# Performance work log

Measured on AMD Instinct MI355X. Metric: run time of the kernel, lower is better.

The kernel has to match this reference:

```python
import jax, jax.numpy as jnp
import numpy as np
from jax import lax

EPS = 1e-5

# ---- 1-bit activation quantizer with straight-through estimator ----
@jax.custom_vjp
def ste_sign(x):
    return jnp.sign(x)

def _ste_sign_fwd(x):
    return jnp.sign(x), x

def _ste_sign_bwd(res, g):
    x = res
    # clipped STE: pass gradient where |x| <= 1
    return (g * (jnp.abs(x) <= 1.0).astype(g.dtype),)

ste_sign.defvjp(_ste_sign_fwd, _ste_sign_bwd)

# ---- 1-bit weight binarization: sign(w) * per-out-channel mean(|w|), STE ----
@jax.custom_vjp
def bin_weight(w):
    alpha = jnp.mean(jnp.abs(w), axis=(1, 2, 3), keepdims=True)  # [O,1,1,1]
    return jnp.sign(w) * alpha

def _bw_fwd(w):
    return bin_weight(w), w

def _bw_bwd(res, g):
    w = res
    # weight_clip=1: straight-through inside the clip range
    return (g * (jnp.abs(w) <= 1.0).astype(g.dtype),)

bin_weight.defvjp(_bw_fwd, _bw_bwd)

def conv3x3(x, w):
    # zero padding=1, stride=1, NCHW / OIHW
    return lax.conv_general_dilated(
        x, w, window_strides=(1, 1), padding=((1, 1), (1, 1)),
        dimension_numbers=('NCHW', 'OIHW', 'NCHW'))

def batchnorm(x, gamma, beta):
    # training-mode BN with batch statistics over (N,H,W)
    mean = jnp.mean(x, axis=(0, 2, 3), keepdims=True)
    var = jnp.var(x, axis=(0, 2, 3), keepdims=True)
    xn = (x - mean) * lax.rsqrt(var + EPS)
    return xn * gamma[None, :, None, None] + beta[None, :, None, None]


def setup_inputs() -> dict:
    key = jax.random.key(0)
    k1, k2, k3 = jax.random.split(key, 3)
    N, C, H, W = 32, 256, 56, 56
    return {
        'x': jax.random.normal(k1, (N, C, H, W), dtype=jnp.float32),
        'w1': jax.random.normal(k2, (C, C, 3, 3), dtype=jnp.float32) * 0.05,
        'gamma1': jnp.ones((C,), dtype=jnp.float32),
        'beta1': jnp.zeros((C,), dtype=jnp.float32),
        'w2': jax.random.normal(k3, (C, C, 3, 3), dtype=jnp.float32) * 0.05,
        'gamma2': jnp.ones((C,), dtype=jnp.float32),
        'beta2': jnp.zeros((C,), dtype=jnp.float32),
    }


def reference(x, w1, gamma1, beta1, w2, gamma2, beta2):
    identity = x
    out = ste_sign(x)                       # quantized activation (1-bit, signed)
    out = conv3x3(out, bin_weight(w1))      # BinConv 3x3, stride 1
    out = batchnorm(out, gamma1, beta1)
    out = ste_sign(out)
    out = conv3x3(out, bin_weight(w2))
    out = batchnorm(out, gamma2, beta2)
    return out + identity                   # residual add (downsample=None)
```

## Files before the change

kernel.cpp:

```cpp
#include <hip/hip_runtime.h>
#include <stdint.h>

#define NB 32
#define CH 256
#define HH 56
#define WW 56
#define HWSZ (HH*WW)
#define NPIX (NB*HWSZ)
#define HP 58
#define WP 58
#define PADPIX (NB*HP*WP)
#define NTAPS 9
#define KKE (CH*NTAPS)
#define NPIXD 100352.0
#define WQ_CONV (NTAPS*8*8*64*16)
#define HSTRIDE 272

typedef int int4v  __attribute__((ext_vector_type(4)));
typedef int int16v __attribute__((ext_vector_type(16)));
typedef unsigned int uint4v __attribute__((ext_vector_type(4)));

__global__ void init_kernel(long long* __restrict__ sums8) {
    int t = blockIdx.x*256 + threadIdx.x;
    if (t < 2*8*512) sums8[t] = 0;
}

__global__ void wqpack_kernel(const float* __restrict__ w1, const float* __restrict__ w2,
                              int8_t* __restrict__ wq) {
    int t = blockIdx.x*256 + threadIdx.x;
    int conv = blockIdx.y;
    const float* w = conv ? w2 : w1;
    int lane = t & 63;
    int g = t >> 6;
    int nb = g & 7, h = g >> 3;
    int ks = h & 7, tap = h >> 3;
    int o = nb*32 + (lane & 31);
    int cin0 = ks*32 + (lane >> 5)*16;
    int wd[4];
    #pragma unroll
    for (int q = 0; q < 4; ++q) {
        int wv = 0;
        #pragma unroll
        for (int j = 0; j < 4; ++j) {
            float v = w[(size_t)(o*CH + cin0 + q*4 + j)*NTAPS + tap];
            int s = (v > 0.f) ? 1 : ((v < 0.f) ? -1 : 0);
            wv |= (s & 0xff) << (8*j);
        }
        wd[q] = wv;
    }
    *(int4v*)(wq + (size_t)conv*WQ_CONV + (size_t)t*16) = (int4v){wd[0], wd[1], wd[2], wd[3]};
}

__global__ void alpha_kernel(const float* __restrict__ w1, const float* __restrict__ w2,
                             float* __restrict__ alpha) {
    int o = blockIdx.x; int conv = blockIdx.y;
    const float* w = conv ? w2 : w1;
    float s = 0.f;
    for (int i = threadIdx.x; i < KKE; i += 256) s += fabsf(w[(size_t)o*KKE + i]);
    for (int off = 32; off; off >>= 1) s += __shfl_down(s, off);
    __shared__ float l[4];
    int lane = threadIdx.x & 63, wv = threadIdx.x >> 6;
    if (lane == 0) l[wv] = s;
    __syncthreads();
    if (threadIdx.x == 0) alpha[conv*CH + o] = (l[0]+l[1]+l[2]+l[3]) * (1.f/KKE);
}

__global__ void pack_x_kernel(const float* __restrict__ x, int8_t* __restrict__ apad) {
    int p = blockIdx.x*256 + threadIdx.x;
    if (p >= PADPIX) return;
    int n  = p / (HP*WP);
    int r  = p - n*(HP*WP);
    int hp = r / WP, wp = r - hp*WP;
    int4v* dst = (int4v*)(apad + (size_t)p*CH);
    if (hp >= 1 && hp <= HH && wp >= 1 && wp <= WW) {
        const float* xb = x + (size_t)n*CH*HWSZ + (hp-1)*WW + (wp-1);
        #pragma unroll 2
        for (int c16 = 0; c16 < 16; ++c16) {
            int wd[4];
            #pragma unroll
            for (int q = 0; q < 4; ++q) {
                int wv = 0;
                #pragma unroll
                for (int j = 0; j < 4; ++j) {
                    float v = xb[(size_t)(c16*16 + q*4 + j)*HWSZ];
                    int s = (v > 0.f) ? 1 : ((v < 0.f) ? -1 : 0);
                    wv |= (s & 0xff) << (8*j);
                }
                wd[q] = wv;
            }
            dst[c16] = (int4v){wd[0], wd[1], wd[2], wd[3]};
        }
    } else {
        int4v z = {0,0,0,0};
        #pragma unroll
        for (int c16 = 0; c16 < 16; ++c16) dst[c16] = z;
    }
}

#define AOFF(IT) (((((IT)>>3)/3)*10 + (((IT)>>3)%3))*HSTRIDE + ((IT)&7)*32)

#define ISSUE_SET(IT) do { \
        int k_ = (IT) % 4; \
        uint32_t ao_ = (uint32_t)AOFF(IT); \
        uint32_t vo_ = voff + (uint32_t)(IT)*8192u; \
        asm volatile("ds_read_b128 %0, %1" : "=v"(as_[k_][0]) : "v"(a0addr + ao_)); \
        asm volatile("ds_read_b128 %0, %1" : "=v"(as_[k_][1]) : "v"(a1addr + ao_)); \
        asm volatile("buffer_load_dwordx4 %0, %1, %2, 0 offen" \
                     : "=v"(bs_[k_][0]) : "v"(vo_), "s"(rsrc)); \
        asm volatile("buffer_load_dwordx4 %0, %1, %2, 0 offen offset:1024" \
                     : "=v"(bs_[k_][1]) : "v"(vo_), "s"(rsrc)); \
    } while (0)

#define CONV_BODY \
    __syncthreads(); \
    int lane = t & 63; \
    int nbp = __builtin_amdgcn_readfirstlane(t >> 6); \
    int kh = lane >> 5, lr = lane & 31; \
    int r0 = lr >> 3, c0 = lr & 7; \
    int base0 = (r0*10 + c0)*HSTRIDE + kh*16; \
    int base1 = base0 + 40*HSTRIDE; \
    uint32_t a0addr = (uint32_t)(uintptr_t)halo + (uint32_t)base0; \
    uint32_t a1addr = (uint32_t)(uintptr_t)halo + (uint32_t)base1; \
    uint32_t voff = (uint32_t)(nbp*2048 + lane*16); \
    uint4v rsrc; \
    { union { const int8_t* p; unsigned long long u; } pu_; pu_.p = wq; \
      rsrc.x = (unsigned)pu_.u; rsrc.y = (unsigned)(pu_.u >> 32); \
      rsrc.z = 0xffffffffu; rsrc.w = 0x00020000u; } \
    int4v as_[4][2], bs_[4][2]; \
    int16v acc00, acc01, acc10, acc11; \
    _Pragma("unroll") \
    for (int i = 0; i < 16; ++i) { acc00[i]=0; acc01[i]=0; acc10[i]=0; acc11[i]=0; } \
    ISSUE_SET(0); \
    ISSUE_SET(1); \
    ISSUE_SET(2); \
    _Pragma("unroll") \
    for (int it = 0; it < 72; ++it) { \
        if (it < 70)       { asm volatile("s_waitcnt lgkmcnt(4) vmcnt(4)"); } \
        else if (it == 70) { asm volatile("s_waitcnt lgkmcnt(2) vmcnt(2)"); } \
        else               { asm volatile("s_waitcnt lgkmcnt(0) vmcnt(0)"); } \
        __builtin_amdgcn_sched_barrier(0); \
        if (it + 3 < 72) { ISSUE_SET(it + 3); } \
        int kc_ = it % 4; \
        acc00 = __builtin_amdgcn_mfma_i32_32x32x32_i8(as_[kc_][0], bs_[kc_][0], acc00, 0,0,0); \
        acc01 = __builtin_amdgcn_mfma_i32_32x32x32_i8(as_[kc_][0], bs_[kc_][1], acc01, 0,0,0); \
        acc10 = __builtin_amdgcn_mfma_i32_32x32x32_i8(as_[kc_][1], bs_[kc_][0], acc10, 0,0,0); \
        acc11 = __builtin_amdgcn_mfma_i32_32x32x32_i8(as_[kc_][1], bs_[kc_][1], acc11, 0,0,0); \
    } \
    { \
        int s1a = 0, s2a = 0, s1b = 0, s2b = 0; \
        _Pragma("unroll") \
        for (int reg = 0; reg < 16; ++reg) { \
            int row_ = (reg & 3) + 8*(reg >> 2) + 4*kh; \
            _Pragma("unroll") \
            for (int m = 0; m < 2; ++m) { \
                int pm_ = m*32 + row_; \
                int rr_ = pm_ >> 3, cc_ = pm_ & 7; \
                size_t pbase_ = (size_t)((n0*HH + ty*8 + rr_)*WW + tx*8 + cc_)*CH; \
                int v0 = (m ? acc10[reg] : acc00[reg]); \
                int v1 = (m ? acc11[reg] : acc01[reg]); \
                cnt[pbase_ + (nbp*2+0)*32 + lr] = (int16_t)v0; \
                cnt[pbase_ + (nbp*2+1)*32 + lr] = (int16_t)v1; \
                s1a += v0; s2a += v0*v0; s1b += v1; s2b += v1*v1; \
            } \
        } \
        s1a += __shfl_down(s1a, 32); s2a += __shfl_down(s2a, 32); \
        s1b += __shfl_down(s1b, 32); s2b += __shfl_down(s2b, 32); \
        if (lane < 32) { \
            long long* sp = sums8 + (size_t)(b & 7)*512; \
            int ch0 = nbp*64 + lr, ch1 = ch0 + 32; \
            atomicAdd((unsigned long long*)&sp[2*ch0],   (unsigned long long)(long long)s1a); \
            atomicAdd((unsigned long long*)&sp[2*ch0+1], (unsigned long long)(long long)s2a); \
            atomicAdd((unsigned long long*)&sp[2*ch1],   (unsigned long long)(long long)s1b); \
            atomicAdd((unsigned long long*)&sp[2*ch1+1], (unsigned long long)(long long)s2b); \
        } \
    }

__global__ __launch_bounds__(256, 3) void conv_kernel(
        const int8_t* __restrict__ apad, const int8_t* __restrict__ wq,
        int16_t* __restrict__ cnt, long long* __restrict__ sums8) {
    __shared__ __attribute__((aligned(16))) int8_t halo[100*HSTRIDE];
    int b = blockIdx.x;
    int tile = b % 49, n0 = b / 49;
    int ty = tile / 7, tx = tile % 7;
    int t = threadIdx.x;

    #pragma unroll 1
    for (int j = 0; j < 7; ++j) {
        int idx = t + j*256;
        if (idx < 1600) {
            int pix = idx >> 4, c16 = idx & 15;
            int dr = pix / 10, dc = pix - dr*10;
            const int4v* src = (const int4v*)(apad +
                ((size_t)((n0*HP + ty*8+dr)*WP + tx*8+dc))*CH + c16*16);
            *(int4v*)&halo[pix*HSTRIDE + c16*16] = *src;
        }
    }
    CONV_BODY
}

__global__ __launch_bounds__(256, 3) void conv2_kernel(
        const int16_t* __restrict__ src16, const float* __restrict__ ab,
        const int8_t* __restrict__ wq,
        int16_t* __restrict__ cnt, long long* __restrict__ sums8) {
    __shared__ __attribute__((aligned(16))) int8_t halo[100*HSTRIDE];
    int b = blockIdx.x;
    int tile = b % 49, n0 = b / 49;
    int ty = tile / 7, tx = tile % 7;
    int t = threadIdx.x;

    {
        int c16s = t & 15;
        #pragma unroll 1
        for (int k = 0; k < 7; ++k) {
            int pix = (t >> 4) + k*16;
            if (pix < 100) {
                int dr = pix / 10, dc = pix - dr*10;
                int hi = ty*8 + dr - 1, wi = tx*8 + dc - 1;
                int4v outv = {0,0,0,0};
                if ((unsigned)hi < (unsigned)HH && (unsigned)wi < (unsigned)WW) {
                    const int16_t* sp = src16 + ((size_t)(n0*HH + hi)*WW + wi)*CH + c16s*16;
                    int4v u0 = *(const int4v*)sp;
                    int4v u1 = *(const int4v*)(sp + 8);
                    int wd[4];
                    #pragma unroll
                    for (int q = 0; q < 4; ++q) {
                        int wv = 0;
                        #pragma unroll
                        for (int j = 0; j < 4; ++j) {
                            int e = q*4 + j;
                            int word = (e < 8) ? u0[e >> 1] : u1[(e-8) >> 1];
                            int sval = (e & 1) ? (word >> 16) : ((word << 16) >> 16);
                            int ch = c16s*16 + e;
                            float v = fmaf(ab[ch], (float)sval, ab[CH + ch]);
                            int s = (v > 0.f) ? 1 : ((v < 0.f) ? -1 : 0);
                            wv |= (s & 0xff) << (8*j);
                        }
                        wd[q] = wv;
                    }
                    outv = (int4v){wd[0], wd[1], wd[2], wd[3]};
                }
                *(int4v*)&halo[pix*HSTRIDE + c16s*16] = outv;
            }
        }
    }
    CONV_BODY
}

__global__ void bncoef_kernel(const long long* __restrict__ sums8,
                              const float* __restrict__ alpha,
                              const float* __restrict__ gamma, const float* __restrict__ beta,
                              float* __restrict__ ab) {
    int o = threadIdx.x;
    long long S1i = 0, S2i = 0;
    #pragma unroll
    for (int k = 0; k < 8; ++k) {
        S1i += sums8[(size_t)k*512 + 2*o];
        S2i += sums8[(size_t)k*512 + 2*o + 1];
    }
    double S1 = (double)S1i, S2 = (double)S2i;
    double mean = S1 / NPIXD;
    double var  = S2 / NPIXD - mean*mean;
    double al   = (double)alpha[o];
    double rs   = 1.0 / sqrt(al*al*var + 1e-5);
    double a    = (double)gamma[o] * al * rs;
    ab[o]      = (float)a;
    ab[CH + o] = (float)((double)beta[o] - a*mean);
}

__global__ __launch_bounds__(256) void final_kernel(const int16_t* __restrict__ cnt,
        const float* __restrict__ x, const float* __restrict__ ab, float* __restrict__ out) {
    __shared__ int4v lsd4[64*32];
    int8_t* lb = (int8_t*)lsd4;
    int b = blockIdx.x;
    int n = b / 49, tile = b - n*49;
    int p0 = tile * 64;
    int t = threadIdx.x;
    const int4v* src = (const int4v*)(cnt + ((size_t)n*HWSZ + p0)*CH);
    #pragma unroll
    for (int j = 0; j < 8; ++j) {
        int c = t + j*256;
        int pix = c >> 5, c16 = c & 31;
        *(int4v*)&lb[pix*512 + ((c16*16) ^ ((pix & 15) << 4))] = src[c];
    }
    __syncthreads();
    int pixL = t & 63;
    int cb = (t >> 6) * 64;
    #pragma unroll 1
    for (int i = 0; i < 8; ++i) {
        int ch0 = cb + i*8;
        int4v v = *(const int4v*)&lb[pixL*512 + ((ch0*2) ^ ((pixL & 15) << 4))];
        #pragma unroll
        for (int j = 0; j < 8; ++j) {
            int ch = ch0 + j;
            int word = v[j >> 1];
            int sval = (j & 1) ? (word >> 16) : ((word << 16) >> 16);
            size_t g = (size_t)(n*CH + ch)*HWSZ + p0 + pixL;
            out[g] = fmaf(ab[ch], (float)sval, ab[CH + ch]) + x[g];
        }
    }
}

extern "C" void kernel_launch(void* const* d_in, const int* in_sizes, int n_in,
                              void* d_out, int out_size, void* d_ws, size_t ws_size,
                              hipStream_t stream) {
    const float* x  = (const float*)d_in[0];
    const float* w1 = (const float*)d_in[1];
    const float* g1 = (const float*)d_in[2];
    const float* b1 = (const float*)d_in[3];
    const float* w2 = (const float*)d_in[4];
    const float* g2 = (const float*)d_in[5];
    const float* b2 = (const float*)d_in[6];
    float* out = (float*)d_out;

    char* ws = (char*)d_ws;
    size_t off = 0;
    auto alloc = [&](size_t nbytes) { char* pp = ws + off; off = (off + nbytes + 255) & ~(size_t)255; return pp; };
    int8_t*   apad  = (int8_t*)alloc((size_t)PADPIX*CH);
    int16_t*  cnt1  = (int16_t*)alloc((size_t)NPIX*CH*2);
    int16_t*  cnt2  = (int16_t*)alloc((size_t)NPIX*CH*2);
    int8_t*   wq    = (int8_t*)alloc((size_t)2*WQ_CONV);
    float*    alpha = (float*)alloc((size_t)2*CH*4);
    long long* sums8 = (long long*)alloc((size_t)2*8*512*8);
    float*    ab    = (float*)alloc((size_t)2*2*CH*4);

    init_kernel<<<32, 256, 0, stream>>>(sums8);
    wqpack_kernel<<<dim3(144, 2), 256, 0, stream>>>(w1, w2, wq);
    alpha_kernel<<<dim3(CH, 2), 256, 0, stream>>>(w1, w2, alpha);
    pack_x_kernel<<<(PADPIX + 255)/256, 256, 0, stream>>>(x, apad);

    conv_kernel<<<1568, 256, 0, stream>>>(apad, wq, cnt1, sums8);
    bncoef_kernel<<<1, CH, 0, stream>>>(sums8, alpha, g1, b1, ab);

    conv2_kernel<<<1568, 256, 0, stream>>>(cnt1, ab, wq + WQ_CONV, cnt2, sums8 + 8*512);
    bncoef_kernel<<<1, CH, 0, stream>>>(sums8 + 8*512, alpha + CH, g2, b2, ab + 2*CH);

    final_kernel<<<1568, 256, 0, stream>>>(cnt2, x, ab + 2*CH, out);
}
```

Baseline: 235.7 us.

## Remap conv warp tile to 32 pixels by 128 channels per wave

Each of the four waves previously computed a 64-pixel by 64-channel tile, two A fragments from LDS times two B fragments from global. Now each wave computes 32 pixels by 128 channels, with one LDS A read and four global B loads per k-step. This halves LDS reads and doubles global weight traffic per wave. It leans on weights being cached in L1/L2, and adds B registers and vmcnt pressure.

Measured after the change: 268.4 us. 13.9% more time.

```diff
diff --git a/kernel.cpp b/kernel.cpp
--- a/kernel.cpp
+++ b/kernel.cpp
@@ -103,75 +103,84 @@
         int k_ = (IT) % 4; \
         uint32_t ao_ = (uint32_t)AOFF(IT); \
         uint32_t vo_ = voff + (uint32_t)(IT)*8192u; \
-        asm volatile("ds_read_b128 %0, %1" : "=v"(as_[k_][0]) : "v"(a0addr + ao_)); \
-        asm volatile("ds_read_b128 %0, %1" : "=v"(as_[k_][1]) : "v"(a1addr + ao_)); \
+        asm volatile("ds_read_b128 %0, %1" : "=v"(as_[k_]) : "v"(a0addr + ao_)); \
         asm volatile("buffer_load_dwordx4 %0, %1, %2, 0 offen" \
                      : "=v"(bs_[k_][0]) : "v"(vo_), "s"(rsrc)); \
         asm volatile("buffer_load_dwordx4 %0, %1, %2, 0 offen offset:1024" \
                      : "=v"(bs_[k_][1]) : "v"(vo_), "s"(rsrc)); \
+        asm volatile("buffer_load_dwordx4 %0, %1, %2, 0 offen offset:2048" \
+                     : "=v"(bs_[k_][2]) : "v"(vo_), "s"(rsrc)); \
+        asm volatile("buffer_load_dwordx4 %0, %1, %2, 0 offen offset:3072" \
+                     : "=v"(bs_[k_][3]) : "v"(vo_), "s"(rsrc)); \
     } while (0)
 
 #define CONV_BODY \
     __syncthreads(); \
     int lane = t & 63; \
-    int nbp = __builtin_amdgcn_readfirstlane(t >> 6); \
+    int wv4 = __builtin_amdgcn_readfirstlane(t >> 6);    \
+    int msub = wv4 & 1;             \
+    int nh   = wv4 >> 1;            \
     int kh = lane >> 5, lr = lane & 31; \
     int r0 = lr >> 3, c0 = lr & 7; \
-    int base0 = (r0*10 + c0)*HSTRIDE + kh*16; \
-    int base1 = base0 + 40*HSTRIDE; \
+    int base0 = ((r0 + msub*4)*10 + c0)*HSTRIDE + kh*16; \
     uint32_t a0addr = (uint32_t)(uintptr_t)halo + (uint32_t)base0; \
-    uint32_t a1addr = (uint32_t)(uintptr_t)halo + (uint32_t)base1; \
-    uint32_t voff = (uint32_t)(nbp*2048 + lane*16); \
+    uint32_t voff = (uint32_t)(nh*4096 + lane*16); \
     uint4v rsrc; \
     { union { const int8_t* p; unsigned long long u; } pu_; pu_.p = wq; \
       rsrc.x = (unsigned)pu_.u; rsrc.y = (unsigned)(pu_.u >> 32); \
       rsrc.z = 0xffffffffu; rsrc.w = 0x00020000u; } \
-    int4v as_[4][2], bs_[4][2]; \
-    int16v acc00, acc01, acc10, acc11; \
+    int4v as_[4], bs_[4][4]; \
+    int16v acc0, acc1, acc2, acc3; \
     _Pragma("unroll") \
-    for (int i = 0; i < 16; ++i) { acc00[i]=0; acc01[i]=0; acc10[i]=0; acc11[i]=0; } \
+    for (int i = 0; i < 16; ++i) { acc0[i]=0; acc1[i]=0; acc2[i]=0; acc3[i]=0; } \
     ISSUE_SET(0); \
     ISSUE_SET(1); \
     ISSUE_SET(2); \
     _Pragma("unroll") \
     for (int it = 0; it < 72; ++it) { \
-        if (it < 70)       { asm volatile("s_waitcnt lgkmcnt(4) vmcnt(4)"); } \
-        else if (it == 70) { asm volatile("s_waitcnt lgkmcnt(2) vmcnt(2)"); } \
+        if (it < 70)       { asm volatile("s_waitcnt lgkmcnt(2) vmcnt(8)"); } \
+        else if (it == 70) { asm volatile("s_waitcnt lgkmcnt(1) vmcnt(4)"); } \
         else               { asm volatile("s_waitcnt lgkmcnt(0) vmcnt(0)"); } \
         __builtin_amdgcn_sched_barrier(0); \
         if (it + 3 < 72) { ISSUE_SET(it + 3); } \
         int kc_ = it % 4; \
-        acc00 = __builtin_amdgcn_mfma_i32_32x32x32_i8(as_[kc_][0], bs_[kc_][0], acc00, 0,0,0); \
-        acc01 = __builtin_amdgcn_mfma_i32_32x32x32_i8(as_[kc_][0], bs_[kc_][1], acc01, 0,0,0); \
-        acc10 = __builtin_amdgcn_mfma_i32_32x32x32_i8(as_[kc_][1], bs_[kc_][0], acc10, 0,0,0); \
-        acc11 = __builtin_amdgcn_mfma_i32_32x32x32_i8(as_[kc_][1], bs_[kc_][1], acc11, 0,0,0); \
+        acc0 = __builtin_amdgcn_mfma_i32_32x32x32_i8(as_[kc_], bs_[kc_][0], acc0, 0,0,0); \
+        acc1 = __builtin_amdgcn_mfma_i32_32x32x32_i8(as_[kc_], bs_[kc_][1], acc1, 0,0,0); \
+        acc2 = __builtin_amdgcn_mfma_i32_32x32x32_i8(as_[kc_], bs_[kc_][2], acc2, 0,0,0); \
+        acc3 = __builtin_amdgcn_mfma_i32_32x32x32_i8(as_[kc_], bs_[kc_][3], acc3, 0,0,0); \
     } \
     { \
-        int s1a = 0, s2a = 0, s1b = 0, s2b = 0; \
+        int s1[4] = {0,0,0,0}, s2[4] = {0,0,0,0}; \
         _Pragma("unroll") \
         for (int reg = 0; reg < 16; ++reg) { \
             int row_ = (reg & 3) + 8*(reg >> 2) + 4*kh; \
+            int pm_ = msub*32 + row_; \
+            int rr_ = pm_ >> 3, cc_ = pm_ & 7; \
+            size_t pbase_ = (size_t)((n0*HH + ty*8 + rr_)*WW + tx*8 + cc_)*CH; \
             _Pragma("unroll") \
-            for (int m = 0; m < 2; ++m) { \
-                int pm_ = m*32 + row_; \
-                int rr_ = pm_ >> 3, cc_ = pm_ & 7; \
-                size_t pbase_ = (size_t)((n0*HH + ty*8 + rr_)*WW + tx*8 + cc_)*CH; \
-                int v0 = (m ? acc10[reg] : acc00[reg]); \
-                int v1 = (m ? acc11[reg] : acc01[reg]); \
-                cnt[pbase_ + (nbp*2+0)*32 + lr] = (int16_t)v0; \
-                cnt[pbase_ + (nbp*2+1)*32 + lr] = (int16_t)v1; \
-                s1a += v0; s2a += v0*v0; s1b += v1; s2b += v1*v1; \
+            for (int j = 0; j < 4; ++j) { \
+                int v_; \
+                if (j == 0)      v_ = acc0[reg]; \
+                else if (j == 1) v_ = acc1[reg]; \
+                else if (j == 2) v_ = acc2[reg]; \
+                else             v_ = acc3[reg]; \
+                cnt[pbase_ + nh*128 + j*32 + lr] = (int16_t)v_; \
+                s1[j] += v_; s2[j] += v_*v_; \
             } \
         } \
-        s1a += __shfl_down(s1a, 32); s2a += __shfl_down(s2a, 32); \
-        s1b += __shfl_down(s1b, 32); s2b += __shfl_down(s2b, 32); \
+        _Pragma("unroll") \
+        for (int j = 0; j < 4; ++j) { \
+            s1[j] += __shfl_down(s1[j], 32); \
+            s2[j] += __shfl_down(s2[j], 32); \
+        } \
         if (lane < 32) { \
             long long* sp = sums8 + (size_t)(b & 7)*512; \
-            int ch0 = nbp*64 + lr, ch1 = ch0 + 32; \
-            atomicAdd((unsigned long long*)&sp[2*ch0],   (unsigned long long)(long long)s1a); \
-            atomicAdd((unsigned long long*)&sp[2*ch0+1], (unsigned long long)(long long)s2a); \
-            atomicAdd((unsigned long long*)&sp[2*ch1],   (unsigned long long)(long long)s1b); \
-            atomicAdd((unsigned long long*)&sp[2*ch1+1], (unsigned long long)(long long)s2b); \
+            _Pragma("unroll") \
+            for (int j = 0; j < 4; ++j) { \
+                int ch_ = nh*128 + j*32 + lr; \
+                atomicAdd((unsigned long long*)&sp[2*ch_],   (unsigned long long)(long long)s1[j]); \
+                atomicAdd((unsigned long long*)&sp[2*ch_+1], (unsigned long long)(long long)s2[j]); \
+            } \
         } \
     }
 
```
